# Optimization experiments

Hardware: AMD Instinct MI355X
Metric: run time of the kernel (lower is better)

Reference implementation:

```python
import jax, jax.numpy as jnp
import numpy as np

B, S, HID = 1, 2048, 2048
H, HKV, D = 16, 8, 128

def _rope_tables(seq_len, dim, base=10000.0):
    inv_freq = 1.0 / (base ** (np.arange(0, dim, 2, dtype=np.float32) / dim))
    t = np.arange(seq_len, dtype=np.float32)
    freqs = np.outer(t, inv_freq)                      # [S, D/2]
    emb = np.concatenate([freqs, freqs], axis=-1)      # [S, D]
    return jnp.asarray(np.cos(emb)), jnp.asarray(np.sin(emb))

def setup_inputs() -> dict:
    key = jax.random.key(0)
    ks = jax.random.split(key, 5)
    x = jax.random.normal(ks[0], (B, S, HID), dtype=jnp.float32)
    Wq = jax.random.normal(ks[1], (H * D, HID), dtype=jnp.float32) * (HID ** -0.5)
    Wk = jax.random.normal(ks[2], (HKV * D, HID), dtype=jnp.float32) * (HID ** -0.5)
    Wv = jax.random.normal(ks[3], (HKV * D, HID), dtype=jnp.float32) * (HID ** -0.5)
    Wo = jax.random.normal(ks[4], (HID, H * D), dtype=jnp.float32) * ((H * D) ** -0.5)
    cos, sin = _rope_tables(S, D)
    return {"x": x, "Wq": Wq, "Wk": Wk, "Wv": Wv, "Wo": Wo, "cos": cos, "sin": sin}

def _rotate_half(t):
    t1, t2 = jnp.split(t, 2, axis=-1)
    return jnp.concatenate([-t2, t1], axis=-1)

def _apply_rope(t, cos, sin):
    # t: [B, h, S, D]; cos/sin: [S, D]
    return t * cos[None, None, :, :] + _rotate_half(t) * sin[None, None, :, :]

def reference(x, Wq, Wk, Wv, Wo, cos, sin):
    b, s, _ = x.shape
    # QKV projections (no bias) + shape to [B, h, S, D]
    q = jnp.einsum('bsh,eh->bse', x, Wq).reshape(b, s, H, D).transpose(0, 2, 1, 3)
    k = jnp.einsum('bsh,eh->bse', x, Wk).reshape(b, s, HKV, D).transpose(0, 2, 1, 3)
    v = jnp.einsum('bsh,eh->bse', x, Wv).reshape(b, s, HKV, D).transpose(0, 2, 1, 3)
    # rotary embedding (rotate-half, non-interleaved)
    q = _apply_rope(q, cos, sin)
    k = _apply_rope(k, cos, sin)
    # GQA: repeat kv heads to match query heads
    rep = H // HKV
    k = jnp.repeat(k, rep, axis=1)
    v = jnp.repeat(v, rep, axis=1)
    scale = D ** -0.5  # attn_scaling is None -> default 1/sqrt(dim_per_head)
    scores = jnp.einsum('bhqd,bhkd->bhqk', q, k) * scale
    causal = jnp.tril(jnp.ones((s, s), dtype=bool))  # decoder causal mask
    scores = jnp.where(causal[None, None, :, :], scores, jnp.finfo(scores.dtype).min)
    attn = jax.nn.softmax(scores, axis=-1)
    ctx = jnp.einsum('bhqk,bhkd->bhqd', attn, v)
    ctx = ctx.transpose(0, 2, 1, 3).reshape(b, s, H * D)  # unshape
    out = jnp.einsum('bse,he->bsh', ctx, Wo)  # final linear, no bias
    return out
```

## Files before the change

### kernel.cpp

```cpp
#include <hip/hip_runtime.h>
#include <hip/hip_bf16.h>

#define S_LEN 2048
#define HIDN  2048
#define NH    16
#define NKV   8
#define DH    128

typedef __bf16 bf16_t;
typedef __bf16 bf16x4 __attribute__((ext_vector_type(4)));
typedef __bf16 bf16x8 __attribute__((ext_vector_type(8)));
typedef float  floatx4 __attribute__((ext_vector_type(4)));

#define NEG_BIG (-1.0e30f)

#define BM 128
#define BN 128
#define BK 64

__device__ __forceinline__ void g2l16(const bf16_t* g, bf16_t* l) {
  __builtin_amdgcn_global_load_lds(
      (const __attribute__((address_space(1))) unsigned int*)g,
      (__attribute__((address_space(3))) unsigned int*)l, 16, 0, 0);
}

__global__ void cvt_all_kernel(const float* __restrict__ x,  const float* __restrict__ wq,
                               const float* __restrict__ wk, const float* __restrict__ wv,
                               const float* __restrict__ wo,
                               bf16_t* __restrict__ xc,  bf16_t* __restrict__ wqc,
                               bf16_t* __restrict__ wkc, bf16_t* __restrict__ wvc,
                               bf16_t* __restrict__ woc)
{
  const int b = blockIdx.x;
  const float* src; bf16_t* dst; int off;
  if      (b < 1024) { src = x;  dst = xc;  off = b; }
  else if (b < 2048) { src = wq; dst = wqc; off = b - 1024; }
  else if (b < 2560) { src = wk; dst = wkc; off = b - 2048; }
  else if (b < 3072) { src = wv; dst = wvc; off = b - 2560; }
  else               { src = wo; dst = woc; off = b - 3072; }
  const int base = off * 4096 + threadIdx.x;
  #pragma unroll
  for (int i = 0; i < 16; ++i)
    dst[base + i * 256] = (bf16_t)src[base + i * 256];
}

__device__ __forceinline__ void gemm_tile(
    const bf16_t* __restrict__ A, const bf16_t* __restrict__ Bt,
    int K, int m0, int n0, floatx4 acc[4][4], bf16_t* As, bf16_t* Bs)
{
  const int tid  = threadIdx.x;
  const int lane = tid & 63;
  const int wave = tid >> 6;
  const int wm = (wave & 1) << 6;
  const int wn = (wave >> 1) << 6;
  const int lr = lane & 15;
  const int lq = lane >> 4;

  #pragma unroll
  for (int i = 0; i < 4; ++i)
    #pragma unroll
    for (int j = 0; j < 4; ++j)
      acc[i][j] = floatx4{0.f, 0.f, 0.f, 0.f};

  for (int k0 = 0; k0 < K; k0 += BK) {
    #pragma unroll
    for (int it = 0; it < 4; ++it) {
      int linear = it * 256 + tid;
      int row = linear >> 3;
      int pc  = linear & 7;
      int c   = pc ^ (row & 7);
      g2l16(A  + (size_t)(m0 + row) * K + k0 + c * 8, As + linear * 8);
      g2l16(Bt + (size_t)(n0 + row) * K + k0 + c * 8, Bs + linear * 8);
    }
    __syncthreads();
    #pragma unroll
    for (int kk = 0; kk < BK; kk += 32) {
      bf16x8 af[4], bfr[4];
      #pragma unroll
      for (int t = 0; t < 4; ++t) {
        int pcr = ((kk >> 3) + lq) ^ (lr & 7);
        af[t]  = *(const bf16x8*)(As + (wm + t * 16 + lr) * BK + pcr * 8);
        bfr[t] = *(const bf16x8*)(Bs + (wn + t * 16 + lr) * BK + pcr * 8);
      }
      #pragma unroll
      for (int i = 0; i < 4; ++i)
        #pragma unroll
        for (int j = 0; j < 4; ++j)
          acc[i][j] = __builtin_amdgcn_mfma_f32_16x16x32_bf16(af[i], bfr[j], acc[i][j], 0, 0, 0);
    }
    __syncthreads();
  }
}

__global__ void __launch_bounds__(256, 2) gemm_qkv_kernel(
    const bf16_t* __restrict__ x, const bf16_t* __restrict__ Wq,
    const bf16_t* __restrict__ Wk, const bf16_t* __restrict__ Wv,
    bf16_t* __restrict__ qb, bf16_t* __restrict__ kb, bf16_t* __restrict__ vb)
{
  __shared__ __align__(16) bf16_t As[BM * BK];
  __shared__ __align__(16) bf16_t Bs[BN * BK];
  const int m0 = blockIdx.x * BM;
  const int nt = blockIdx.y;
  const bf16_t* Bt;
  bf16_t* outp;
  int hbase;
  if (nt < 16)      { Bt = Wq + (size_t)nt * 128 * HIDN;        outp = qb; hbase = nt; }
  else if (nt < 24) { Bt = Wk + (size_t)(nt - 16) * 128 * HIDN; outp = kb; hbase = nt - 16; }
  else              { Bt = Wv + (size_t)(nt - 24) * 128 * HIDN; outp = vb; hbase = nt - 24; }

  floatx4 acc[4][4];
  gemm_tile(x, Bt, HIDN, m0, 0, acc, As, Bs);

  const int lane = threadIdx.x & 63, wave = threadIdx.x >> 6;
  const int wm = (wave & 1) << 6, wn = (wave >> 1) << 6;
  const int lr = lane & 15, lq = lane >> 4;
  #pragma unroll
  for (int i = 0; i < 4; ++i)
    #pragma unroll
    for (int j = 0; j < 4; ++j)
      #pragma unroll
      for (int r = 0; r < 4; ++r) {
        int srow = m0 + wm + i * 16 + lq * 4 + r;
        int d    = wn + j * 16 + lr;
        outp[((size_t)hbase * S_LEN + srow) * DH + d] = (bf16_t)acc[i][j][r];
      }
}

__global__ void __launch_bounds__(256, 2) gemm_out_kernel(
    const bf16_t* __restrict__ ctx, const bf16_t* __restrict__ Wo,
    float* __restrict__ out)
{
  __shared__ __align__(16) bf16_t As[BM * BK];
  __shared__ __align__(16) bf16_t Bs[BN * BK];
  const int m0 = blockIdx.x * BM;
  const int n0 = blockIdx.y * BN;
  floatx4 acc[4][4];
  gemm_tile(ctx, Wo, HIDN, m0, n0, acc, As, Bs);

  const int lane = threadIdx.x & 63, wave = threadIdx.x >> 6;
  const int wm = (wave & 1) << 6, wn = (wave >> 1) << 6;
  const int lr = lane & 15, lq = lane >> 4;
  #pragma unroll
  for (int i = 0; i < 4; ++i)
    #pragma unroll
    for (int j = 0; j < 4; ++j)
      #pragma unroll
      for (int r = 0; r < 4; ++r) {
        int srow = m0 + wm + i * 16 + lq * 4 + r;
        int col  = n0 + wn + j * 16 + lr;
        out[(size_t)srow * HIDN + col] = acc[i][j][r];
      }
}

__global__ void rope_vtrans_kernel(bf16_t* __restrict__ qb, bf16_t* __restrict__ kb,
                                   const float* __restrict__ cosT, const float* __restrict__ sinT,
                                   const bf16_t* __restrict__ vb, bf16_t* __restrict__ vtb)
{
  const int b = blockIdx.x;
  if (b < 12288) {
    const int NQ = NH * S_LEN * 64;
    int idx = b * 256 + threadIdx.x;
    bf16_t* base = qb;
    int rem = idx;
    if (idx >= NQ) { base = kb; rem = idx - NQ; }
    int d  = rem & 63;
    int s  = (rem >> 6) & (S_LEN - 1);
    int hh = rem >> 17;
    size_t off = ((size_t)hh * S_LEN + s) * DH;
    float c  = cosT[s * DH + d];
    float sn = sinT[s * DH + d];
    float a  = (float)base[off + d];
    float bb = (float)base[off + d + 64];
    base[off + d]      = (bf16_t)(a * c - bb * sn);
    base[off + d + 64] = (bf16_t)(bb * c + a * sn);
  } else {
    __shared__ bf16_t tile[64][65];
    const int idx = b - 12288;
    const int hkv = idx >> 6;
    const int rem = idx & 63;
    const int s0 = (rem >> 1) * 64;
    const int d0 = (rem & 1) * 64;
    const int r = threadIdx.x >> 2;
    const int c = (threadIdx.x & 3) * 16;
    const bf16_t* src = vb + (size_t)hkv * S_LEN * DH;
    #pragma unroll
    for (int u = 0; u < 16; ++u)
      tile[r][c + u] = src[(size_t)(s0 + r) * DH + d0 + c + u];
    __syncthreads();
    bf16_t* dst = vtb + (size_t)hkv * DH * S_LEN;
    #pragma unroll
    for (int u = 0; u < 16; ++u)
      dst[(size_t)(d0 + r) * S_LEN + s0 + c + u] = tile[c + u][r];
  }
}

#define PSTR 144
__global__ void __launch_bounds__(256, 1) attn_kernel(
    const bf16_t* __restrict__ qb, const bf16_t* __restrict__ kb,
    const bf16_t* __restrict__ vtb, bf16_t* __restrict__ ctx)
{
  __shared__ __align__(16) bf16_t Kb[2][128 * 128];
  __shared__ __align__(16) bf16_t Vb[2][128 * 128];
  __shared__ __align__(16) bf16_t Pb[4][16 * PSTR];

  const int tid  = threadIdx.x;
  const int lane = tid & 63, wave = tid >> 6;
  const int lr   = lane & 15, quad = lane >> 4;

  const int h   = blockIdx.x >> 4;
  const int w   = blockIdx.x & 15;
  const int hkv = h >> 1;

  const bf16_t* kbase  = kb  + (size_t)hkv * S_LEN * DH;
  const bf16_t* vtbase = vtb + (size_t)hkv * DH * S_LEN;
  const float scale = 0.08838834764831845f;
  bf16_t* pmine = &Pb[wave][0];

  auto stage = [&](int cc, int buf) {
    const int kv0 = cc * 128;
    #pragma unroll
    for (int it = 0; it < 8; ++it) {
      int linear = it * 256 + tid;
      int row = linear >> 4;
      int pc  = linear & 15;
      int c   = pc ^ (row & 15);
      g2l16(kbase  + (size_t)(kv0 + row) * DH + c * 8,  &Kb[buf][linear * 8]);
      g2l16(vtbase + (size_t)row * S_LEN + kv0 + c * 8, &Vb[buf][linear * 8]);
    }
  };

  for (int tt = 0; tt < 2; ++tt) {
    const int qt  = tt ? (31 - w) : w;
    const int q0  = qt * 64;
    const int nch = (qt >> 1) + 1;
    const int qrow_g = q0 + wave * 16 + lr;

    const bf16_t* qrp = qb + ((size_t)h * S_LEN + qrow_g) * DH;
    bf16x8 qf[4];
    #pragma unroll
    for (int kk = 0; kk < 4; ++kk)
      qf[kk] = *(const bf16x8*)(qrp + kk * 32 + quad * 8);

    float m_r = NEG_BIG, l_r = 0.f;
    floatx4 o[8];
    #pragma unroll
    for (int t = 0; t < 8; ++t) o[t] = floatx4{0.f, 0.f, 0.f, 0.f};

    stage(0, 0);

    for (int cc = 0; cc < nch; ++cc) {
      const int buf = cc & 1;
      __syncthreads();
      if (cc + 1 < nch) stage(cc + 1, buf ^ 1);
      const int kv0 = cc * 128;

      floatx4 sacc[8];
      #pragma unroll
      for (int t = 0; t < 8; ++t) sacc[t] = floatx4{0.f, 0.f, 0.f, 0.f};
      #pragma unroll
      for (int kk = 0; kk < 4; ++kk) {
        const int pc = ((kk << 2) + quad) ^ lr;
        #pragma unroll
        for (int t = 0; t < 8; ++t) {
          bf16x8 kf = *(const bf16x8*)(&Kb[buf][(t * 16 + lr) * 128 + pc * 8]);
          sacc[t] = __builtin_amdgcn_mfma_f32_16x16x32_bf16(kf, qf[kk], sacc[t], 0, 0, 0);
        }
      }

      if (cc == nch - 1) {
        #pragma unroll
        for (int t = 0; t < 8; ++t)
          #pragma unroll
          for (int r = 0; r < 4; ++r) {
            int kv = kv0 + t * 16 + quad * 4 + r;
            if (kv > qrow_g) sacc[t][r] = NEG_BIG;
          }
      }

      float mx = sacc[0][0];
      #pragma unroll
      for (int t = 0; t < 8; ++t)
        #pragma unroll
        for (int r = 0; r < 4; ++r) mx = fmaxf(mx, sacc[t][r]);
      mx = fmaxf(mx, __shfl_xor(mx, 16, 64));
      mx = fmaxf(mx, __shfl_xor(mx, 32, 64));
      const float mn = fmaxf(m_r, mx * scale);
      const float alpha = __expf(m_r - mn);

      float lc = 0.f;
      #pragma unroll
      for (int t = 0; t < 8; ++t) {
        bf16x4 pk;
        #pragma unroll
        for (int r = 0; r < 4; ++r) {
          float p = __expf(fmaf(sacc[t][r], scale, -mn));
          lc += p;
          pk[r] = (bf16_t)p;
        }
        *(bf16x4*)(pmine + lr * PSTR + t * 16 + quad * 4) = pk;
      }
      lc += __shfl_xor(lc, 16, 64);
      lc += __shfl_xor(lc, 32, 64);
      l_r = l_r * alpha + lc;
      m_r = mn;

      #pragma unroll
      for (int t = 0; t < 8; ++t)
        #pragma unroll
        for (int r = 0; r < 4; ++r) o[t][r] *= alpha;
      #pragma unroll
      for (int ks = 0; ks < 4; ++ks) {
        bf16x8 pf = *(const bf16x8*)(pmine + lr * PSTR + ks * 32 + quad * 8);
        const int pc = ((ks << 2) + quad) ^ lr;
        #pragma unroll
        for (int t = 0; t < 8; ++t) {
          bf16x8 vf = *(const bf16x8*)(&Vb[buf][(t * 16 + lr) * 128 + pc * 8]);
          o[t] = __builtin_amdgcn_mfma_f32_16x16x32_bf16(vf, pf, o[t], 0, 0, 0);
        }
      }
    }

    __syncthreads();
    const float inv = 1.0f / l_r;
    bf16_t* crow = ctx + (size_t)qrow_g * HIDN + h * DH;
    #pragma unroll
    for (int t = 0; t < 8; ++t) {
      bf16x4 ov;
      #pragma unroll
      for (int r = 0; r < 4; ++r) ov[r] = (bf16_t)(o[t][r] * inv);
      *(bf16x4*)(crow + t * 16 + quad * 4) = ov;
    }
  }
}

extern "C" void kernel_launch(void* const* d_in, const int* in_sizes, int n_in,
                              void* d_out, int out_size, void* d_ws, size_t ws_size,
                              hipStream_t stream)
{
  const float* xf   = (const float*)d_in[0];
  const float* Wqf  = (const float*)d_in[1];
  const float* Wkf  = (const float*)d_in[2];
  const float* Wvf  = (const float*)d_in[3];
  const float* Wof  = (const float*)d_in[4];
  const float* cosT = (const float*)d_in[5];
  const float* sinT = (const float*)d_in[6];
  float* out = (float*)d_out;

  char* ws = (char*)d_ws;
  const size_t MB = 1u << 20;
  bf16_t* xc  = (bf16_t*)(ws);
  bf16_t* Wqc = (bf16_t*)(ws + 8  * MB);
  bf16_t* Wkc = (bf16_t*)(ws + 16 * MB);
  bf16_t* Wvc = (bf16_t*)(ws + 20 * MB);
  bf16_t* Woc = (bf16_t*)(ws + 24 * MB);
  bf16_t* qb  = (bf16_t*)(ws + 32 * MB);
  bf16_t* kb  = (bf16_t*)(ws + 40 * MB);
  bf16_t* vb  = (bf16_t*)(ws + 44 * MB);
  bf16_t* vtb = (bf16_t*)(ws + 48 * MB);
  bf16_t* ctx = (bf16_t*)(ws + 52 * MB);

  hipLaunchKernelGGL(cvt_all_kernel, dim3(4096), dim3(256), 0, stream,
                     xf, Wqf, Wkf, Wvf, Wof, xc, Wqc, Wkc, Wvc, Woc);
  hipLaunchKernelGGL(gemm_qkv_kernel, dim3(16, 32), dim3(256), 0, stream,
                     xc, Wqc, Wkc, Wvc, qb, kb, vb);
  hipLaunchKernelGGL(rope_vtrans_kernel, dim3(12800), dim3(256), 0, stream,
                     qb, kb, cosT, sinT, vb, vtb);
  hipLaunchKernelGGL(attn_kernel, dim3(256), dim3(256), 0, stream,
                     qb, kb, vtb, ctx);
  hipLaunchKernelGGL(gemm_out_kernel, dim3(16, 16), dim3(256), 0, stream,
                     ctx, Woc, out);
}
```

Baseline: 251.8 us.

## Fuse RoPE and V transpose into QKV GEMM epilogue; retile attention to 64-key chunks

The QKV GEMM now stages its output tile in shared memory and applies rotary embedding to Q/K, or writes V transposed, directly in the epilogue. This removes the separate rope/transpose kernel and its extra global round-trip. The attention kernel switches to 64-wide KV chunks with smaller LDS buffers and one q-tile per block across 512 blocks. The launch bound allows two blocks per CU. The added epilogue LDS buffer raises GEMM shared-memory use, and the transposed V stores stride through memory.

```diff
diff --git a/kernel.cpp b/kernel.cpp
--- a/kernel.cpp
+++ b/kernel.cpp
@@ -95,23 +95,25 @@
 __global__ void __launch_bounds__(256, 2) gemm_qkv_kernel(
     const bf16_t* __restrict__ x, const bf16_t* __restrict__ Wq,
     const bf16_t* __restrict__ Wk, const bf16_t* __restrict__ Wv,
-    bf16_t* __restrict__ qb, bf16_t* __restrict__ kb, bf16_t* __restrict__ vb)
+    bf16_t* __restrict__ qb, bf16_t* __restrict__ kb, bf16_t* __restrict__ vtb,
+    const float* __restrict__ cosT, const float* __restrict__ sinT)
 {
   __shared__ __align__(16) bf16_t As[BM * BK];
   __shared__ __align__(16) bf16_t Bs[BN * BK];
+  __shared__ __align__(16) bf16_t Epi[128 * 132];
+  const int tid = threadIdx.x;
   const int m0 = blockIdx.x * BM;
   const int nt = blockIdx.y;
   const bf16_t* Bt;
-  bf16_t* outp;
   int hbase;
-  if (nt < 16)      { Bt = Wq + (size_t)nt * 128 * HIDN;        outp = qb; hbase = nt; }
-  else if (nt < 24) { Bt = Wk + (size_t)(nt - 16) * 128 * HIDN; outp = kb; hbase = nt - 16; }
-  else              { Bt = Wv + (size_t)(nt - 24) * 128 * HIDN; outp = vb; hbase = nt - 24; }
+  if (nt < 16)      { Bt = Wq + (size_t)nt * 128 * HIDN;        hbase = nt; }
+  else if (nt < 24) { Bt = Wk + (size_t)(nt - 16) * 128 * HIDN; hbase = nt - 16; }
+  else              { Bt = Wv + (size_t)(nt - 24) * 128 * HIDN; hbase = nt - 24; }
 
   floatx4 acc[4][4];
   gemm_tile(x, Bt, HIDN, m0, 0, acc, As, Bs);
 
-  const int lane = threadIdx.x & 63, wave = threadIdx.x >> 6;
+  const int lane = tid & 63, wave = tid >> 6;
   const int wm = (wave & 1) << 6, wn = (wave >> 1) << 6;
   const int lr = lane & 15, lq = lane >> 4;
   #pragma unroll
@@ -120,10 +122,36 @@
     for (int j = 0; j < 4; ++j)
       #pragma unroll
       for (int r = 0; r < 4; ++r) {
-        int srow = m0 + wm + i * 16 + lq * 4 + r;
-        int d    = wn + j * 16 + lr;
-        outp[((size_t)hbase * S_LEN + srow) * DH + d] = (bf16_t)acc[i][j][r];
-      }
+        int row = wm + i * 16 + lq * 4 + r;
+        int col = wn + j * 16 + lr;
+        Epi[row * 132 + col] = (bf16_t)acc[i][j][r];
+      }
+  __syncthreads();
+
+  if (nt < 24) {
+    bf16_t* outp = (nt < 16) ? qb : kb;
+    #pragma unroll
+    for (int u = 0; u < 32; ++u) {
+      int idx = u * 256 + tid;
+      int dd = idx & 63, s = idx >> 6;
+      float a = (float)Epi[s * 132 + dd];
+      float b = (float)Epi[s * 132 + dd + 64];
+      int sg = m0 + s;
+      float cv = cosT[sg * DH + dd];
+      float sv = sinT[sg * DH + dd];
+      size_t off = ((size_t)hbase * S_LEN + sg) * DH;
+      outp[off + dd]      = (bf16_t)(a * cv - b * sv);
+      outp[off + dd + 64] = (bf16_t)(b * cv + a * sv);
+    }
+  } else {
+    bf16_t* dst = vtb + (size_t)hbase * DH * S_LEN;
+    #pragma unroll
+    for (int u = 0; u < 64; ++u) {
+      int idx = u * 256 + tid;
+      int sl = idx & 127, d = idx >> 7;
+      dst[(size_t)d * S_LEN + m0 + sl] = Epi[sl * 132 + d];
+    }
+  }
 }
 
 __global__ void __launch_bounds__(256, 2) gemm_out_kernel(
@@ -152,184 +180,141 @@
       }
 }
 
-__global__ void rope_vtrans_kernel(bf16_t* __restrict__ qb, bf16_t* __restrict__ kb,
-                                   const float* __restrict__ cosT, const float* __restrict__ sinT,
-                                   const bf16_t* __restrict__ vb, bf16_t* __restrict__ vtb)
-{
-  const int b = blockIdx.x;
-  if (b < 12288) {
-    const int NQ = NH * S_LEN * 64;
-    int idx = b * 256 + threadIdx.x;
-    bf16_t* base = qb;
-    int rem = idx;
-    if (idx >= NQ) { base = kb; rem = idx - NQ; }
-    int d  = rem & 63;
-    int s  = (rem >> 6) & (S_LEN - 1);
-    int hh = rem >> 17;
-    size_t off = ((size_t)hh * S_LEN + s) * DH;
-    float c  = cosT[s * DH + d];
-    float sn = sinT[s * DH + d];
-    float a  = (float)base[off + d];
-    float bb = (float)base[off + d + 64];
-    base[off + d]      = (bf16_t)(a * c - bb * sn);
-    base[off + d + 64] = (bf16_t)(bb * c + a * sn);
-  } else {
-    __shared__ bf16_t tile[64][65];
-    const int idx = b - 12288;
-    const int hkv = idx >> 6;
-    const int rem = idx & 63;
-    const int s0 = (rem >> 1) * 64;
-    const int d0 = (rem & 1) * 64;
-    const int r = threadIdx.x >> 2;
-    const int c = (threadIdx.x & 3) * 16;
-    const bf16_t* src = vb + (size_t)hkv * S_LEN * DH;
-    #pragma unroll
-    for (int u = 0; u < 16; ++u)
-      tile[r][c + u] = src[(size_t)(s0 + r) * DH + d0 + c + u];
-    __syncthreads();
-    bf16_t* dst = vtb + (size_t)hkv * DH * S_LEN;
-    #pragma unroll
-    for (int u = 0; u < 16; ++u)
-      dst[(size_t)(d0 + r) * S_LEN + s0 + c + u] = tile[c + u][r];
-  }
-}
-
-#define PSTR 144
-__global__ void __launch_bounds__(256, 1) attn_kernel(
+__global__ void __launch_bounds__(256, 2) attn_kernel(
     const bf16_t* __restrict__ qb, const bf16_t* __restrict__ kb,
     const bf16_t* __restrict__ vtb, bf16_t* __restrict__ ctx)
 {
-  __shared__ __align__(16) bf16_t Kb[2][128 * 128];
-  __shared__ __align__(16) bf16_t Vb[2][128 * 128];
-  __shared__ __align__(16) bf16_t Pb[4][16 * PSTR];
+  __shared__ __align__(16) bf16_t Kb[2][64 * 128];
+  __shared__ __align__(16) bf16_t Vb[2][128 * 64];
+  __shared__ __align__(16) bf16_t Pb[4][16 * 64];
 
   const int tid  = threadIdx.x;
   const int lane = tid & 63, wave = tid >> 6;
   const int lr   = lane & 15, quad = lane >> 4;
 
-  const int h   = blockIdx.x >> 4;
-  const int w   = blockIdx.x & 15;
+  const int b = blockIdx.x;
+  int h, qt;
+  if (b < 256) { h = b >> 5;              qt = b & 31; }
+  else         { int c = b - 256; h = 8 + (c >> 5); qt = 31 - (c & 31); }
   const int hkv = h >> 1;
+  const int q0  = qt * 64;
+  const int nch = qt + 1;
+  const int qrow_g = q0 + wave * 16 + lr;
 
   const bf16_t* kbase  = kb  + (size_t)hkv * S_LEN * DH;
   const bf16_t* vtbase = vtb + (size_t)hkv * DH * S_LEN;
   const float scale = 0.08838834764831845f;
   bf16_t* pmine = &Pb[wave][0];
 
+  const bf16_t* qrp = qb + ((size_t)h * S_LEN + qrow_g) * DH;
+  bf16x8 qf[4];
+  #pragma unroll
+  for (int kk = 0; kk < 4; ++kk)
+    qf[kk] = *(const bf16x8*)(qrp + kk * 32 + quad * 8);
+
   auto stage = [&](int cc, int buf) {
-    const int kv0 = cc * 128;
-    #pragma unroll
-    for (int it = 0; it < 8; ++it) {
+    const int kv0 = cc * 64;
+    #pragma unroll
+    for (int it = 0; it < 4; ++it) {
       int linear = it * 256 + tid;
-      int row = linear >> 4;
-      int pc  = linear & 15;
-      int c   = pc ^ (row & 15);
-      g2l16(kbase  + (size_t)(kv0 + row) * DH + c * 8,  &Kb[buf][linear * 8]);
-      g2l16(vtbase + (size_t)row * S_LEN + kv0 + c * 8, &Vb[buf][linear * 8]);
+      int krow = linear >> 4, kpc = linear & 15;
+      int kc = kpc ^ (krow & 15);
+      g2l16(kbase + (size_t)(kv0 + krow) * DH + kc * 8, &Kb[buf][linear * 8]);
+      int vrow = linear >> 3, vpc = linear & 7;
+      int vc = vpc ^ (vrow & 7);
+      g2l16(vtbase + (size_t)vrow * S_LEN + kv0 + vc * 8, &Vb[buf][linear * 8]);
     }
   };
 
-  for (int tt = 0; tt < 2; ++tt) {
-    const int qt  = tt ? (31 - w) : w;
-    const int q0  = qt * 64;
-    const int nch = (qt >> 1) + 1;
-    const int qrow_g = q0 + wave * 16 + lr;
-
-    const bf16_t* qrp = qb + ((size_t)h * S_LEN + qrow_g) * DH;
-    bf16x8 qf[4];
-    #pragma unroll
-    for (int kk = 0; kk < 4; ++kk)
-      qf[kk] = *(const bf16x8*)(qrp + kk * 32 + quad * 8);
-
-    float m_r = NEG_BIG, l_r = 0.f;
-    floatx4 o[8];
-    #pragma unroll
-    for (int t = 0; t < 8; ++t) o[t] = floatx4{0.f, 0.f, 0.f, 0.f};
-
-    stage(0, 0);
-
-    for (int cc = 0; cc < nch; ++cc) {
-      const int buf = cc & 1;
-      __syncthreads();
-      if (cc + 1 < nch) stage(cc + 1, buf ^ 1);
-      const int kv0 = cc * 128;
-
-      floatx4 sacc[8];
-      #pragma unroll
-      for (int t = 0; t < 8; ++t) sacc[t] = floatx4{0.f, 0.f, 0.f, 0.f};
-      #pragma unroll
-      for (int kk = 0; kk < 4; ++kk) {
-        const int pc = ((kk << 2) + quad) ^ lr;
-        #pragma unroll
-        for (int t = 0; t < 8; ++t) {
-          bf16x8 kf = *(const bf16x8*)(&Kb[buf][(t * 16 + lr) * 128 + pc * 8]);
-          sacc[t] = __builtin_amdgcn_mfma_f32_16x16x32_bf16(kf, qf[kk], sacc[t], 0, 0, 0);
-        }
-      }
-
-      if (cc == nch - 1) {
-        #pragma unroll
-        for (int t = 0; t < 8; ++t)
-          #pragma unroll
-          for (int r = 0; r < 4; ++r) {
-            int kv = kv0 + t * 16 + quad * 4 + r;
-            if (kv > qrow_g) sacc[t][r] = NEG_BIG;
-          }
-      }
-
-      float mx = sacc[0][0];
-      #pragma unroll
-      for (int t = 0; t < 8; ++t)
-        #pragma unroll
-        for (int r = 0; r < 4; ++r) mx = fmaxf(mx, sacc[t][r]);
-      mx = fmaxf(mx, __shfl_xor(mx, 16, 64));
-      mx = fmaxf(mx, __shfl_xor(mx, 32, 64));
-      const float mn = fmaxf(m_r, mx * scale);
-      const float alpha = __expf(m_r - mn);
-
-      float lc = 0.f;
-      #pragma unroll
-      for (int t = 0; t < 8; ++t) {
-        bf16x4 pk;
+  float m_r = NEG_BIG, l_r = 0.f;
+  floatx4 o[8];
+  #pragma unroll
+  for (int t = 0; t < 8; ++t) o[t] = floatx4{0.f, 0.f, 0.f, 0.f};
+
+  stage(0, 0);
+
+  for (int cc = 0; cc < nch; ++cc) {
+    const int buf = cc & 1;
+    __syncthreads();
+    if (cc + 1 < nch) stage(cc + 1, buf ^ 1);
+    const int kv0 = cc * 64;
+
+    floatx4 sacc[4];
+    #pragma unroll
+    for (int t = 0; t < 4; ++t) sacc[t] = floatx4{0.f, 0.f, 0.f, 0.f};
+    #pragma unroll
+    for (int kk = 0; kk < 4; ++kk) {
+      const int pc = ((kk << 2) + quad) ^ lr;
+      #pragma unroll
+      for (int t = 0; t < 4; ++t) {
+        bf16x8 kf = *(const bf16x8*)(&Kb[buf][(t * 16 + lr) * 128 + pc * 8]);
+        sacc[t] = __builtin_amdgcn_mfma_f32_16x16x32_bf16(kf, qf[kk], sacc[t], 0, 0, 0);
+      }
+    }
+
+    if (cc == nch - 1) {
+      #pragma unroll
+      for (int t = 0; t < 4; ++t)
         #pragma unroll
         for (int r = 0; r < 4; ++r) {
-          float p = __expf(fmaf(sacc[t][r], scale, -mn));
-          lc += p;
-          pk[r] = (bf16_t)p;
+          int kv = kv0 + t * 16 + quad * 4 + r;
+          if (kv > qrow_g) sacc[t][r] = NEG_BIG;
         }
-        *(bf16x4*)(pmine + lr * PSTR + t * 16 + quad * 4) = pk;
-      }
-      lc += __shfl_xor(lc, 16, 64);
-      lc += __shfl_xor(lc, 32, 64);
-      l_r = l_r * alpha + lc;
-      m_r = mn;
-
-      #pragma unroll
-      for (int t = 0; t < 8; ++t)
-        #pragma unroll
-        for (int r = 0; r < 4; ++r) o[t][r] *= alpha;
-      #pragma unroll
-      for (int ks = 0; ks < 4; ++ks) {
-        bf16x8 pf = *(const bf16x8*)(pmine + lr * PSTR + ks * 32 + quad * 8);
-        const int pc = ((ks << 2) + quad) ^ lr;
-        #pragma unroll
-        for (int t = 0; t < 8; ++t) {
-          bf16x8 vf = *(const bf16x8*)(&Vb[buf][(t * 16 + lr) * 128 + pc * 8]);
-          o[t] = __builtin_amdgcn_mfma_f32_16x16x32_bf16(vf, pf, o[t], 0, 0, 0);
-        }
-      }
-    }
-
-    __syncthreads();
-    const float inv = 1.0f / l_r;
-    bf16_t* crow = ctx + (size_t)qrow_g * HIDN + h * DH;
-    #pragma unroll
-    for (int t = 0; t < 8; ++t) {
-      bf16x4 ov;
-      #pragma unroll
-      for (int r = 0; r < 4; ++r) ov[r] = (bf16_t)(o[t][r] * inv);
-      *(bf16x4*)(crow + t * 16 + quad * 4) = ov;
-    }
+    }
+
+    float mx = sacc[0][0];
+    #pragma unroll
+    for (int t = 0; t < 4; ++t)
+      #pragma unroll
+      for (int r = 0; r < 4; ++r) mx = fmaxf(mx, sacc[t][r]);
+    mx = fmaxf(mx, __shfl_xor(mx, 16, 64));
+    mx = fmaxf(mx, __shfl_xor(mx, 32, 64));
+    const float mn = fmaxf(m_r, mx * scale);
+    const float alpha = __expf(m_r - mn);
+
+    float lc = 0.f;
+    #pragma unroll
+    for (int t = 0; t < 4; ++t) {
+      bf16x4 pk;
+      #pragma unroll
+      for (int r = 0; r < 4; ++r) {
+        float p = __expf(fmaf(sacc[t][r], scale, -mn));
+        lc += p;
+        pk[r] = (bf16_t)p;
+      }
+      int pw = lr * 64 + (((2 * t + (quad >> 1)) ^ (lr & 7)) << 3) + (quad & 1) * 4;
+      *(bf16x4*)(pmine + pw) = pk;
+    }
+    lc += __shfl_xor(lc, 16, 64);
+    lc += __shfl_xor(lc, 32, 64);
+    l_r = l_r * alpha + lc;
+    m_r = mn;
+
+    #pragma unroll
+    for (int t = 0; t < 8; ++t)
+      #pragma unroll
+      for (int r = 0; r < 4; ++r) o[t][r] *= alpha;
+    #pragma unroll
+    for (int ks = 0; ks < 2; ++ks) {
+      int prd = lr * 64 + (((ks * 4 + quad) ^ (lr & 7)) << 3);
+      bf16x8 pf = *(const bf16x8*)(pmine + prd);
+      #pragma unroll
+      for (int t = 0; t < 8; ++t) {
+        int pc = (ks * 4 + quad) ^ (lr & 7);
+        bf16x8 vf = *(const bf16x8*)(&Vb[buf][(t * 16 + lr) * 64 + pc * 8]);
+        o[t] = __builtin_amdgcn_mfma_f32_16x16x32_bf16(vf, pf, o[t], 0, 0, 0);
+      }
+    }
+  }
+
+  const float inv = 1.0f / l_r;
+  bf16_t* crow = ctx + (size_t)qrow_g * HIDN + h * DH;
+  #pragma unroll
+  for (int t = 0; t < 8; ++t) {
+    bf16x4 ov;
+    #pragma unroll
+    for (int r = 0; r < 4; ++r) ov[r] = (bf16_t)(o[t][r] * inv);
+    *(bf16x4*)(crow + t * 16 + quad * 4) = ov;
   }
 }
 
@@ -355,17 +340,14 @@
   bf16_t* Woc = (bf16_t*)(ws + 24 * MB);
   bf16_t* qb  = (bf16_t*)(ws + 32 * MB);
   bf16_t* kb  = (bf16_t*)(ws + 40 * MB);
-  bf16_t* vb  = (bf16_t*)(ws + 44 * MB);
-  bf16_t* vtb = (bf16_t*)(ws + 48 * MB);
-  bf16_t* ctx = (bf16_t*)(ws + 52 * MB);
+  bf16_t* vtb = (bf16_t*)(ws + 44 * MB);
+  bf16_t* ctx = (bf16_t*)(ws + 48 * MB);
 
   hipLaunchKernelGGL(cvt_all_kernel, dim3(4096), dim3(256), 0, stream,
                      xf, Wqf, Wkf, Wvf, Wof, xc, Wqc, Wkc, Wvc, Woc);
   hipLaunchKernelGGL(gemm_qkv_kernel, dim3(16, 32), dim3(256), 0, stream,
-                     xc, Wqc, Wkc, Wvc, qb, kb, vb);
-  hipLaunchKernelGGL(rope_vtrans_kernel, dim3(12800), dim3(256), 0, stream,
-                     qb, kb, cosT, sinT, vb, vtb);
-  hipLaunchKernelGGL(attn_kernel, dim3(256), dim3(256), 0, stream,
+                     xc, Wqc, Wkc, Wvc, qb, kb, vtb, cosT, sinT);
+  hipLaunchKernelGGL(attn_kernel, dim3(512), dim3(256), 0, stream,
                      qb, kb, vtb, ctx);
   hipLaunchKernelGGL(gemm_out_kernel, dim3(16, 16), dim3(256), 0, stream,
                      ctx, Woc, out);
```

New measurement: 237.9 us. 1.06x faster.
